# Kernel tuning notes

Hardware: AMD Instinct MI355X
Metric: run time of the kernel (lower is better)

## Reference

```python
import jax, jax.numpy as jnp
import numpy as np

# Earth4D config (matches init_kwargs)
L_SPATIAL = 16
L_TEMPORAL = 16
FEAT = 2
LOG2_T = 19
TABLE = 1 << LOG2_T            # 524288 entries per level (power of 2)
BASE_S = 32.0
BASE_T = 32.0
GROWTH = 2.0
N_PTS = 131072

_CORNERS = np.array([[i, j, k] for i in (0, 1) for j in (0, 1) for k in (0, 1)], dtype=np.int32)  # [8,3]


def _encode3d(x, tables, base, growth):
    """Multi-resolution hash-grid encoding (torch-ngp / instant-ngp math).
    x: [N,3] in [0,1]; tables: [L, TABLE, FEAT]. Returns [N, L*FEAT]."""
    L, T, F = tables.shape
    corners = jnp.asarray(_CORNERS)  # [8,3]
    outs = []
    for l in range(L):  # static loop over levels (L=16)
        res = int(np.floor(base * growth ** l))
        pos = x * res                      # [N,3]
        pos_floor = jnp.floor(pos)
        w = pos - pos_floor                # fractional part, [N,3]
        base_idx = pos_floor.astype(jnp.int32)
        c = base_idx[:, None, :] + corners[None]   # [N,8,3] corner grid coords
        if (res + 1) ** 3 <= T:
            # coarse level: dense (stride) indexing, no collisions
            s = res + 1
            idx = c[..., 0] + c[..., 1] * s + c[..., 2] * s * s  # [N,8]
        else:
            # fine level: spatial hash with instant-ngp primes
            cu = c.astype(jnp.uint32)
            h = (cu[..., 0] * jnp.uint32(1)) ^ (cu[..., 1] * jnp.uint32(2654435761)) ^ (cu[..., 2] * jnp.uint32(805459861))
            idx = (h & jnp.uint32(T - 1)).astype(jnp.int32)      # [N,8]
        feats = tables[l][idx]             # gather, [N,8,F]
        # trilinear weights: prod over dims of (w if corner==1 else 1-w)
        wts = jnp.prod(jnp.where(corners[None] == 1, w[:, None, :], 1.0 - w[:, None, :]), axis=-1)  # [N,8]
        outs.append(jnp.einsum('ncf,nc->nf', feats, wts.astype(feats.dtype)))
    return jnp.concatenate(outs, axis=-1)  # [N, L*F]


def setup_inputs() -> dict:
    key = jax.random.key(0)
    k0, k1, k2, k3, k4 = jax.random.split(key, 5)
    xyzt = jax.random.uniform(k0, (N_PTS, 4), dtype=jnp.float32)  # normalized coords in [0,1]
    init = lambda k, L: jax.random.uniform(k, (L, TABLE, FEAT), dtype=jnp.float32, minval=-1e-4, maxval=1e-4)
    return {
        'xyzt': xyzt,
        'spatial_tables': init(k1, L_SPATIAL),
        'xyt_tables': init(k2, L_TEMPORAL),
        'yzt_tables': init(k3, L_TEMPORAL),
        'xzt_tables': init(k4, L_TEMPORAL),
    }


def reference(xyzt, spatial_tables, xyt_tables, yzt_tables, xzt_tables):
    x, y, z, t = xyzt[:, 0], xyzt[:, 1], xyzt[:, 2], xyzt[:, 3]
    xyz = xyzt[:, :3]
    xyt = jnp.stack([x, y, t], axis=-1)
    yzt = jnp.stack([y, z, t], axis=-1)
    xzt = jnp.stack([x, z, t], axis=-1)
    f_xyz = _encode3d(xyz, spatial_tables, BASE_S, GROWTH)   # [N, 32]
    f_xyt = _encode3d(xyt, xyt_tables, BASE_T, GROWTH)       # [N, 32]
    f_yzt = _encode3d(yzt, yzt_tables, BASE_T, GROWTH)       # [N, 32]
    f_xzt = _encode3d(xzt, xzt_tables, BASE_T, GROWTH)       # [N, 32]
    return jnp.concatenate([f_xyz, f_xyt, f_yzt, f_xzt], axis=-1)  # [N, 128]
```

## Files before the change

kernel.cpp:

```cpp
#include <hip/hip_runtime.h>

#define N_PTS 131072
#define LOG2_T 19
#define TABLE_SIZE (1u << LOG2_T)
#define HASH_MASK (TABLE_SIZE - 1u)

typedef float f32x2 __attribute__((ext_vector_type(2)));
typedef float f32x4 __attribute__((ext_vector_type(4)));
typedef _Float16 h16x2 __attribute__((ext_vector_type(2)));
typedef _Float16 h16x4 __attribute__((ext_vector_type(4)));

#define FSCALE 512.0f
#define INV_FSCALE (1.0f / 512.0f)

__global__ __launch_bounds__(256) void earth4d_convert(
    const float* __restrict__ t0, const float* __restrict__ t1,
    const float* __restrict__ t2, const float* __restrict__ t3,
    h16x4* __restrict__ dst)
{
    const float* srcs[4] = {t0, t1, t2, t3};
    unsigned tid = blockIdx.x * 256u + threadIdx.x;
    #pragma unroll
    for (int it = 0; it < 8; ++it) {
        unsigned q = tid + (unsigned)it * 2097152u;
        const f32x4* src = reinterpret_cast<const f32x4*>(srcs[q >> 22]);
        f32x4 v = __builtin_nontemporal_load(src + (q & 0x3FFFFFu));
        h16x4 h = { (_Float16)(v.x * FSCALE), (_Float16)(v.y * FSCALE),
                    (_Float16)(v.z * FSCALE), (_Float16)(v.w * FSCALE) };
        dst[q] = h;
    }
}

template <int MODE>
__global__ __launch_bounds__(256, 2) void earth4d_gather(
    const float* __restrict__ xyzt,
    const float* __restrict__ tab_xyz,
    const float* __restrict__ tab_xyt,
    const float* __restrict__ tab_yzt,
    const float* __restrict__ tab_xzt,
    const h16x2* __restrict__ tab16,
    float* __restrict__ out,
    f32x2* __restrict__ stage)
{
    unsigned b     = blockIdx.x;
    unsigned xcd   = b & 7u;
    unsigned i     = b >> 3;
    unsigned combo = ((i >> 7) << 3) | xcd;
    unsigned chunk = i & 127u;
    unsigned e     = combo >> 4;
    unsigned l     = combo & 15u;

    const float* tab;
    switch (e) {
      case 0:  tab = tab_xyz; break;
      case 1:  tab = tab_xyt; break;
      case 2:  tab = tab_yzt; break;
      default: tab = tab_xzt; break;
    }
    const f32x2* tl32 = reinterpret_cast<const f32x2*>(tab) + (size_t)l * TABLE_SIZE;
    const h16x2* tl16 = tab16 + (size_t)combo * TABLE_SIZE;

    unsigned resu = 32u << l;
    float res = (float)resu;

    unsigned nbase = (chunk << 10) | threadIdx.x;

    float w0[4], w1[4], w2[4];
    unsigned idx[4][8];

    #pragma unroll
    for (int k = 0; k < 4; ++k) {
        unsigned n = nbase + (unsigned)k * 256u;
        float4 p = reinterpret_cast<const float4*>(xyzt)[n];
        float c0, c1, c2;
        switch (e) {
          case 0:  c0 = p.x; c1 = p.y; c2 = p.z; break;
          case 1:  c0 = p.x; c1 = p.y; c2 = p.w; break;
          case 2:  c0 = p.y; c1 = p.z; c2 = p.w; break;
          default: c0 = p.x; c1 = p.z; c2 = p.w; break;
        }
        float p0 = c0 * res, p1 = c1 * res, p2 = c2 * res;
        float f0 = floorf(p0), f1 = floorf(p1), f2 = floorf(p2);
        w0[k] = p0 - f0; w1[k] = p1 - f1; w2[k] = p2 - f2;
        int b0 = (int)f0, b1 = (int)f1, b2 = (int)f2;

        if (l < 2u) {
            int s = (int)resu + 1;
            #pragma unroll
            for (int c = 0; c < 8; ++c) {
                int i0 = b0 + ((c >> 2) & 1);
                int i1 = b1 + ((c >> 1) & 1);
                int i2 = b2 + (c & 1);
                idx[k][c] = (unsigned)(i0 + i1 * s + i2 * s * s);
            }
        } else {
            #pragma unroll
            for (int c = 0; c < 8; ++c) {
                unsigned i0 = (unsigned)(b0 + ((c >> 2) & 1));
                unsigned i1 = (unsigned)(b1 + ((c >> 1) & 1));
                unsigned i2 = (unsigned)(b2 + (c & 1));
                idx[k][c] = (i0 * 1u ^ i1 * 2654435761u ^ i2 * 805459861u) & HASH_MASK;
            }
        }
    }

    float r0[4], r1[4];
    if (MODE == 0) {
        h16x2 v[4][8];
        #pragma unroll
        for (int k = 0; k < 4; ++k)
            #pragma unroll
            for (int c = 0; c < 8; ++c)
                v[k][c] = tl16[idx[k][c]];
        #pragma unroll
        for (int k = 0; k < 4; ++k) {
            float a0 = 0.f, a1 = 0.f;
            #pragma unroll
            for (int c = 0; c < 8; ++c) {
                float wt = ((c & 4) ? w0[k] : 1.f - w0[k])
                         * ((c & 2) ? w1[k] : 1.f - w1[k])
                         * ((c & 1) ? w2[k] : 1.f - w2[k]);
                a0 = fmaf((float)v[k][c].x, wt, a0);
                a1 = fmaf((float)v[k][c].y, wt, a1);
            }
            r0[k] = a0 * INV_FSCALE;
            r1[k] = a1 * INV_FSCALE;
        }
    } else {
        f32x2 v[4][8];
        #pragma unroll
        for (int k = 0; k < 4; ++k)
            #pragma unroll
            for (int c = 0; c < 8; ++c)
                v[k][c] = tl32[idx[k][c]];
        #pragma unroll
        for (int k = 0; k < 4; ++k) {
            float a0 = 0.f, a1 = 0.f;
            #pragma unroll
            for (int c = 0; c < 8; ++c) {
                float wt = ((c & 4) ? w0[k] : 1.f - w0[k])
                         * ((c & 2) ? w1[k] : 1.f - w1[k])
                         * ((c & 1) ? w2[k] : 1.f - w2[k]);
                a0 = fmaf(v[k][c].x, wt, a0);
                a1 = fmaf(v[k][c].y, wt, a1);
            }
            r0[k] = a0;
            r1[k] = a1;
        }
    }

    #pragma unroll
    for (int k = 0; k < 4; ++k) {
        unsigned n = nbase + (unsigned)k * 256u;
        f32x2 r = { r0[k], r1[k] };
        if (MODE != 2) {
            __builtin_nontemporal_store(r, stage + (size_t)combo * N_PTS + n);
        } else {
            __builtin_nontemporal_store(
                r, reinterpret_cast<f32x2*>(out + (size_t)n * 128u + combo * 2u));
        }
    }
}

__global__ __launch_bounds__(256) void earth4d_transpose(
    const f32x2* __restrict__ ws, float* __restrict__ out)
{
    __shared__ f32x2 lds[64][65];
    unsigned n0 = blockIdx.x * 64u;
    unsigned t = threadIdx.x;

    #pragma unroll
    for (int it = 0; it < 16; ++it) {
        unsigned i = (unsigned)it * 256u + t;
        unsigned c = i >> 6;
        unsigned p = i & 63u;
        lds[p][c] = __builtin_nontemporal_load(ws + (size_t)c * N_PTS + n0 + p);
    }
    __syncthreads();

    #pragma unroll
    for (int it = 0; it < 8; ++it) {
        unsigned i = (unsigned)it * 256u + t;
        unsigned p = i >> 5;
        unsigned q = i & 31u;
        f32x2 a = lds[p][2u * q];
        f32x2 b = lds[p][2u * q + 1u];
        f32x4 v = { a.x, a.y, b.x, b.y };
        __builtin_nontemporal_store(
            v, reinterpret_cast<f32x4*>(out + (size_t)(n0 + p) * 128u) + q);
    }
}

extern "C" void kernel_launch(void* const* d_in, const int* in_sizes, int n_in,
                              void* d_out, int out_size, void* d_ws, size_t ws_size,
                              hipStream_t stream) {
    const float* xyzt    = (const float*)d_in[0];
    const float* tab_xyz = (const float*)d_in[1];
    const float* tab_xyt = (const float*)d_in[2];
    const float* tab_yzt = (const float*)d_in[3];
    const float* tab_xzt = (const float*)d_in[4];
    float* out = (float*)d_out;

    const size_t TAB16 = (size_t)64 * TABLE_SIZE * sizeof(h16x2);
    const size_t STAGE = (size_t)64 * N_PTS * sizeof(f32x2);
    dim3 block(256u), grid1(8192u);

    if (d_ws && ws_size >= TAB16 + STAGE) {
        h16x2* tab16 = (h16x2*)d_ws;
        f32x2* stage = (f32x2*)((char*)d_ws + TAB16);
        earth4d_convert<<<dim3(8192u), block, 0, stream>>>(
            tab_xyz, tab_xyt, tab_yzt, tab_xzt, (h16x4*)tab16);
        earth4d_gather<0><<<grid1, block, 0, stream>>>(
            xyzt, tab_xyz, tab_xyt, tab_yzt, tab_xzt, tab16, out, stage);
        earth4d_transpose<<<dim3(N_PTS / 64u), block, 0, stream>>>(stage, out);
    } else if (d_ws && ws_size >= STAGE) {
        f32x2* stage = (f32x2*)d_ws;
        earth4d_gather<1><<<grid1, block, 0, stream>>>(
            xyzt, tab_xyz, tab_xyt, tab_yzt, tab_xzt, (const h16x2*)nullptr, out, stage);
        earth4d_transpose<<<dim3(N_PTS / 64u), block, 0, stream>>>(stage, out);
    } else {
        earth4d_gather<2><<<grid1, block, 0, stream>>>(
            xyzt, tab_xyz, tab_xyt, tab_yzt, tab_xzt, (const h16x2*)nullptr, out, (f32x2*)nullptr);
    }
}
```

Before: 358.5 us.

## Fuse fp16 table conversion and gather into one producer-consumer kernel

Replaces the separate fp32-to-fp16 table-conversion kernel and gather kernel with a single persistent kernel. The first 256 blocks convert table levels and bump per-level completion counters. The remaining blocks spin-wait on those counters and then gather and interpolate. Producers and consumers of a level are mapped to the same XCD so the converted table can be served from that XCD's L2. This is meant to overlap conversion traffic with gathering and remove a kernel boundary, at the cost of spin-waiting, relaxed-ordering visibility risks and fewer resident gather blocks.

```diff
diff --git a/kernel.cpp b/kernel.cpp
--- a/kernel.cpp
+++ b/kernel.cpp
@@ -13,32 +13,139 @@
 #define FSCALE 512.0f
 #define INV_FSCALE (1.0f / 512.0f)
 
-__global__ __launch_bounds__(256) void earth4d_convert(
-    const float* __restrict__ t0, const float* __restrict__ t1,
-    const float* __restrict__ t2, const float* __restrict__ t3,
-    h16x4* __restrict__ dst)
-{
-    const float* srcs[4] = {t0, t1, t2, t3};
-    unsigned tid = blockIdx.x * 256u + threadIdx.x;
-    #pragma unroll
-    for (int it = 0; it < 8; ++it) {
-        unsigned q = tid + (unsigned)it * 2097152u;
-        const f32x4* src = reinterpret_cast<const f32x4*>(srcs[q >> 22]);
-        f32x4 v = __builtin_nontemporal_load(src + (q & 0x3FFFFFu));
-        h16x4 h = { (_Float16)(v.x * FSCALE), (_Float16)(v.y * FSCALE),
-                    (_Float16)(v.z * FSCALE), (_Float16)(v.w * FSCALE) };
-        dst[q] = h;
-    }
-}
-
-template <int MODE>
-__global__ __launch_bounds__(256, 2) void earth4d_gather(
+__global__ __launch_bounds__(256) void earth4d_fused(
     const float* __restrict__ xyzt,
     const float* __restrict__ tab_xyz,
     const float* __restrict__ tab_xyt,
     const float* __restrict__ tab_yzt,
     const float* __restrict__ tab_xzt,
-    const h16x2* __restrict__ tab16,
+    h16x2* __restrict__ tab16,
+    f32x2* __restrict__ stage,
+    unsigned* __restrict__ done)
+{
+    unsigned bid = blockIdx.x;
+    unsigned xcd = bid & 7u;
+
+    if (bid < 256u) {
+        unsigned slice = bid >> 3;
+        for (unsigned j = 0; j < 8u; ++j) {
+            unsigned c = (j << 3) | xcd;
+            unsigned e = c >> 4, l = c & 15u;
+            const float* tab;
+            switch (e) {
+              case 0:  tab = tab_xyz; break;
+              case 1:  tab = tab_xyt; break;
+              case 2:  tab = tab_yzt; break;
+              default: tab = tab_xzt; break;
+            }
+            const f32x4* src = reinterpret_cast<const f32x4*>(tab + (size_t)l * TABLE_SIZE * 2u);
+            h16x4* dq = reinterpret_cast<h16x4*>(tab16 + (size_t)c * TABLE_SIZE);
+            unsigned base_q = slice * 8192u + threadIdx.x;
+            #pragma unroll 8
+            for (int it = 0; it < 32; ++it) {
+                unsigned q = base_q + (unsigned)it * 256u;
+                f32x4 v = __builtin_nontemporal_load(src + q);
+                h16x4 hv = { (_Float16)(v.x * FSCALE), (_Float16)(v.y * FSCALE),
+                             (_Float16)(v.z * FSCALE), (_Float16)(v.w * FSCALE) };
+                dq[q] = hv;
+            }
+            asm volatile("s_waitcnt vmcnt(0)" ::: "memory");
+            if (threadIdx.x == 0)
+                __hip_atomic_fetch_add(&done[c], 1u, __ATOMIC_RELAXED,
+                                       __HIP_MEMORY_SCOPE_AGENT);
+        }
+        return;
+    }
+
+    unsigned g = (bid - 256u) >> 3;
+    for (unsigned vb = g; vb < 1024u; vb += 224u) {
+        unsigned j     = vb >> 7;
+        unsigned chunk = vb & 127u;
+        unsigned combo = (j << 3) | xcd;
+        unsigned e     = combo >> 4;
+        unsigned l     = combo & 15u;
+
+        while (__hip_atomic_load(&done[combo], __ATOMIC_RELAXED,
+                                 __HIP_MEMORY_SCOPE_AGENT) < 32u)
+            __builtin_amdgcn_s_sleep(32);
+
+        const h16x2* tl16 = tab16 + (size_t)combo * TABLE_SIZE;
+
+        unsigned resu = 32u << l;
+        float res = (float)resu;
+        unsigned nbase = (chunk << 10) | threadIdx.x;
+
+        float w0[4], w1[4], w2[4];
+        unsigned idx[4][8];
+
+        #pragma unroll
+        for (int k = 0; k < 4; ++k) {
+            unsigned n = nbase + (unsigned)k * 256u;
+            float4 p = reinterpret_cast<const float4*>(xyzt)[n];
+            float c0, c1, c2;
+            switch (e) {
+              case 0:  c0 = p.x; c1 = p.y; c2 = p.z; break;
+              case 1:  c0 = p.x; c1 = p.y; c2 = p.w; break;
+              case 2:  c0 = p.y; c1 = p.z; c2 = p.w; break;
+              default: c0 = p.x; c1 = p.z; c2 = p.w; break;
+            }
+            float p0 = c0 * res, p1 = c1 * res, p2 = c2 * res;
+            float f0 = floorf(p0), f1 = floorf(p1), f2 = floorf(p2);
+            w0[k] = p0 - f0; w1[k] = p1 - f1; w2[k] = p2 - f2;
+            int b0 = (int)f0, b1 = (int)f1, b2 = (int)f2;
+
+            if (l < 2u) {
+                int s = (int)resu + 1;
+                #pragma unroll
+                for (int c = 0; c < 8; ++c) {
+                    int i0 = b0 + ((c >> 2) & 1);
+                    int i1 = b1 + ((c >> 1) & 1);
+                    int i2 = b2 + (c & 1);
+                    idx[k][c] = (unsigned)(i0 + i1 * s + i2 * s * s);
+                }
+            } else {
+                #pragma unroll
+                for (int c = 0; c < 8; ++c) {
+                    unsigned i0 = (unsigned)(b0 + ((c >> 2) & 1));
+                    unsigned i1 = (unsigned)(b1 + ((c >> 1) & 1));
+                    unsigned i2 = (unsigned)(b2 + (c & 1));
+                    idx[k][c] = (i0 * 1u ^ i1 * 2654435761u ^ i2 * 805459861u) & HASH_MASK;
+                }
+            }
+        }
+
+        h16x2 v[4][8];
+        #pragma unroll
+        for (int k = 0; k < 4; ++k)
+            #pragma unroll
+            for (int c = 0; c < 8; ++c)
+                v[k][c] = tl16[idx[k][c]];
+
+        #pragma unroll
+        for (int k = 0; k < 4; ++k) {
+            float a0 = 0.f, a1 = 0.f;
+            #pragma unroll
+            for (int c = 0; c < 8; ++c) {
+                float wt = ((c & 4) ? w0[k] : 1.f - w0[k])
+                         * ((c & 2) ? w1[k] : 1.f - w1[k])
+                         * ((c & 1) ? w2[k] : 1.f - w2[k]);
+                a0 = fmaf((float)v[k][c].x, wt, a0);
+                a1 = fmaf((float)v[k][c].y, wt, a1);
+            }
+            unsigned n = nbase + (unsigned)k * 256u;
+            f32x2 r = { a0 * INV_FSCALE, a1 * INV_FSCALE };
+            __builtin_nontemporal_store(r, stage + (size_t)combo * N_PTS + n);
+        }
+    }
+}
+
+template <int MODE>
+__global__ __launch_bounds__(256, 2) void earth4d_gather32(
+    const float* __restrict__ xyzt,
+    const float* __restrict__ tab_xyz,
+    const float* __restrict__ tab_xyt,
+    const float* __restrict__ tab_yzt,
+    const float* __restrict__ tab_xzt,
     float* __restrict__ out,
     f32x2* __restrict__ stage)
 {
@@ -58,11 +165,9 @@
       default: tab = tab_xzt; break;
     }
     const f32x2* tl32 = reinterpret_cast<const f32x2*>(tab) + (size_t)l * TABLE_SIZE;
-    const h16x2* tl16 = tab16 + (size_t)combo * TABLE_SIZE;
 
     unsigned resu = 32u << l;
     float res = (float)resu;
-
     unsigned nbase = (chunk << 10) | threadIdx.x;
 
     float w0[4], w1[4], w2[4];
@@ -104,56 +209,27 @@
         }
     }
 
-    float r0[4], r1[4];
-    if (MODE == 0) {
-        h16x2 v[4][8];
-        #pragma unroll
-        for (int k = 0; k < 4; ++k)
-            #pragma unroll
-            for (int c = 0; c < 8; ++c)
-                v[k][c] = tl16[idx[k][c]];
-        #pragma unroll
-        for (int k = 0; k < 4; ++k) {
-            float a0 = 0.f, a1 = 0.f;
-            #pragma unroll
-            for (int c = 0; c < 8; ++c) {
-                float wt = ((c & 4) ? w0[k] : 1.f - w0[k])
-                         * ((c & 2) ? w1[k] : 1.f - w1[k])
-                         * ((c & 1) ? w2[k] : 1.f - w2[k]);
-                a0 = fmaf((float)v[k][c].x, wt, a0);
-                a1 = fmaf((float)v[k][c].y, wt, a1);
-            }
-            r0[k] = a0 * INV_FSCALE;
-            r1[k] = a1 * INV_FSCALE;
-        }
-    } else {
-        f32x2 v[4][8];
-        #pragma unroll
-        for (int k = 0; k < 4; ++k)
-            #pragma unroll
-            for (int c = 0; c < 8; ++c)
-                v[k][c] = tl32[idx[k][c]];
-        #pragma unroll
-        for (int k = 0; k < 4; ++k) {
-            float a0 = 0.f, a1 = 0.f;
-            #pragma unroll
-            for (int c = 0; c < 8; ++c) {
-                float wt = ((c & 4) ? w0[k] : 1.f - w0[k])
-                         * ((c & 2) ? w1[k] : 1.f - w1[k])
-                         * ((c & 1) ? w2[k] : 1.f - w2[k]);
-                a0 = fmaf(v[k][c].x, wt, a0);
-                a1 = fmaf(v[k][c].y, wt, a1);
-            }
-            r0[k] = a0;
-            r1[k] = a1;
-        }
-    }
+    f32x2 v[4][8];
+    #pragma unroll
+    for (int k = 0; k < 4; ++k)
+        #pragma unroll
+        for (int c = 0; c < 8; ++c)
+            v[k][c] = tl32[idx[k][c]];
 
     #pragma unroll
     for (int k = 0; k < 4; ++k) {
+        float a0 = 0.f, a1 = 0.f;
+        #pragma unroll
+        for (int c = 0; c < 8; ++c) {
+            float wt = ((c & 4) ? w0[k] : 1.f - w0[k])
+                     * ((c & 2) ? w1[k] : 1.f - w1[k])
+                     * ((c & 1) ? w2[k] : 1.f - w2[k]);
+            a0 = fmaf(v[k][c].x, wt, a0);
+            a1 = fmaf(v[k][c].y, wt, a1);
+        }
         unsigned n = nbase + (unsigned)k * 256u;
-        f32x2 r = { r0[k], r1[k] };
-        if (MODE != 2) {
+        f32x2 r = { a0, a1 };
+        if (MODE == 1) {
             __builtin_nontemporal_store(r, stage + (size_t)combo * N_PTS + n);
         } else {
             __builtin_nontemporal_store(
@@ -203,23 +279,24 @@
 
     const size_t TAB16 = (size_t)64 * TABLE_SIZE * sizeof(h16x2);
     const size_t STAGE = (size_t)64 * N_PTS * sizeof(f32x2);
-    dim3 block(256u), grid1(8192u);
-
-    if (d_ws && ws_size >= TAB16 + STAGE) {
-        h16x2* tab16 = (h16x2*)d_ws;
-        f32x2* stage = (f32x2*)((char*)d_ws + TAB16);
-        earth4d_convert<<<dim3(8192u), block, 0, stream>>>(
-            tab_xyz, tab_xyt, tab_yzt, tab_xzt, (h16x4*)tab16);
-        earth4d_gather<0><<<grid1, block, 0, stream>>>(
-            xyzt, tab_xyz, tab_xyt, tab_yzt, tab_xzt, tab16, out, stage);
+    const size_t FLAGS = 64 * sizeof(unsigned);
+    dim3 block(256u);
+
+    if (d_ws && ws_size >= TAB16 + STAGE + FLAGS) {
+        h16x2* tab16    = (h16x2*)d_ws;
+        f32x2* stage    = (f32x2*)((char*)d_ws + TAB16);
+        unsigned* flags = (unsigned*)((char*)d_ws + TAB16 + STAGE);
+        hipMemsetAsync(flags, 0, FLAGS, stream);
+        earth4d_fused<<<dim3(2048u), block, 0, stream>>>(
+            xyzt, tab_xyz, tab_xyt, tab_yzt, tab_xzt, tab16, stage, flags);
         earth4d_transpose<<<dim3(N_PTS / 64u), block, 0, stream>>>(stage, out);
     } else if (d_ws && ws_size >= STAGE) {
         f32x2* stage = (f32x2*)d_ws;
-        earth4d_gather<1><<<grid1, block, 0, stream>>>(
-            xyzt, tab_xyz, tab_xyt, tab_yzt, tab_xzt, (const h16x2*)nullptr, out, stage);
+        earth4d_gather32<1><<<dim3(8192u), block, 0, stream>>>(
+            xyzt, tab_xyz, tab_xyt, tab_yzt, tab_xzt, out, stage);
         earth4d_transpose<<<dim3(N_PTS / 64u), block, 0, stream>>>(stage, out);
     } else {
-        earth4d_gather<2><<<grid1, block, 0, stream>>>(
-            xyzt, tab_xyz, tab_xyt, tab_yzt, tab_xzt, (const h16x2*)nullptr, out, (f32x2*)nullptr);
+        earth4d_gather32<2><<<dim3(8192u), block, 0, stream>>>(
+            xyzt, tab_xyz, tab_xyt, tab_yzt, tab_xzt, out, (f32x2*)nullptr);
     }
 }
```

Result: slower. 611.0 us (+70.4%).
